# Kernel tuning notes

Hardware: AMD Instinct MI355X
Metric: run time of the kernel (lower is better)

## Reference

```python
import jax, jax.numpy as jnp
import numpy as np

EPS = 1e-6  # flax LayerNorm default

def _layer_norm(x, scale, bias):
    mu = jnp.mean(x, axis=-1, keepdims=True)
    var = jnp.mean(jnp.square(x - mu), axis=-1, keepdims=True)
    return (x - mu) * jax.lax.rsqrt(var + EPS) * scale + bias

def setup_inputs() -> dict:
    key = jax.random.key(0)
    ks = jax.random.split(key, 8)
    B, S, D_in, D_h, D_out, N = 4, 2048, 1024, 2048, 1024, 6
    init = lambda k, shape, fan_in: jax.random.normal(k, shape, jnp.float32) / np.sqrt(fan_in)
    return {
        "x": jax.random.normal(ks[0], (B, S, D_in), jnp.float32),
        "ln1_scale": jnp.ones((D_in,), jnp.float32),
        "ln1_bias": jnp.zeros((D_in,), jnp.float32),
        "w1": init(ks[1], (D_in, D_h), D_in),
        "b1": jnp.zeros((D_h,), jnp.float32),
        "block_ln_scales": jnp.ones((N, D_h), jnp.float32),
        "block_ln_biases": jnp.zeros((N, D_h), jnp.float32),
        "block_ws": init(ks[2], (N, D_h, D_h), D_h),
        "block_bs": jnp.zeros((N, D_h), jnp.float32),
        "ln2_scale": jnp.ones((D_h,), jnp.float32),
        "ln2_bias": jnp.zeros((D_h,), jnp.float32),
        "w2": init(ks[3], (D_h, D_out), D_h),
        "b2": jnp.zeros((D_out,), jnp.float32),
    }

def reference(x, ln1_scale, ln1_bias, w1, b1, block_ln_scales, block_ln_biases,
              block_ws, block_bs, ln2_scale, ln2_bias, w2, b2):
    # stem: LN -> Linear -> SiLU
    h = _layer_norm(x, ln1_scale, ln1_bias)
    h = jax.nn.silu(jnp.einsum('bsd,dh->bsh', h, w1) + b1)

    # residual blocks via scan over stacked params
    def block(h, params):
        s, b, w, lb = params
        y = _layer_norm(h, s, b)
        y = jax.nn.silu(jnp.einsum('bsh,hk->bsk', y, w) + lb)
        return h + y, None

    h, _ = jax.lax.scan(block, h, (block_ln_scales, block_ln_biases, block_ws, block_bs))

    # head: LN -> Linear
    h = _layer_norm(h, ln2_scale, ln2_bias)
    return jnp.einsum('bsh,ho->bso', h, w2) + b2
```

## Files before the change

kernel.cpp:

```cpp
#include <hip/hip_runtime.h>
#include <hip/hip_bf16.h>

typedef short short8 __attribute__((ext_vector_type(8)));
typedef float f32x4 __attribute__((ext_vector_type(4)));

#define AS1(p) ((const __attribute__((address_space(1))) void*)(p))
#define AS3(p) ((__attribute__((address_space(3))) void*)(p))

__device__ __forceinline__ ushort f2bf(float f) {
  __hip_bfloat16 h = __float2bfloat16(f);
  return *reinterpret_cast<const ushort*>(&h);
}
__device__ __forceinline__ float bfu2f(ushort u) {
  unsigned int x = ((unsigned int)u) << 16;
  float f;
  __builtin_memcpy(&f, &x, 4);
  return f;
}
__device__ __forceinline__ float silu_f(float v) { return v / (1.f + __expf(-v)); }

template<int NV>
__global__ __launch_bounds__(256) void ln_bf16_k(
    const float* __restrict__ in, const float* __restrict__ sc,
    const float* __restrict__ bi, ushort* __restrict__ out)
{
  const int D = NV * 1024;
  const long row = blockIdx.x;
  const int tx = threadIdx.x;
  const float* p = in + row * (long)D;
  float4 v[NV];
  float s = 0.f, s2 = 0.f;
#pragma unroll
  for (int t = 0; t < NV; ++t) {
    v[t] = *reinterpret_cast<const float4*>(p + t * 1024 + tx * 4);
    s  += v[t].x + v[t].y + v[t].z + v[t].w;
    s2 += v[t].x * v[t].x + v[t].y * v[t].y + v[t].z * v[t].z + v[t].w * v[t].w;
  }
#pragma unroll
  for (int o = 1; o < 64; o <<= 1) { s += __shfl_xor(s, o); s2 += __shfl_xor(s2, o); }
  __shared__ float red[2][4];
  const int wave = tx >> 6;
  if ((tx & 63) == 0) { red[0][wave] = s; red[1][wave] = s2; }
  __syncthreads();
  s  = red[0][0] + red[0][1] + red[0][2] + red[0][3];
  s2 = red[1][0] + red[1][1] + red[1][2] + red[1][3];
  const float mu   = s / D;
  const float rstd = rsqrtf(s2 / D - mu * mu + 1e-6f);
#pragma unroll
  for (int t = 0; t < NV; ++t) {
    const int d = t * 1024 + tx * 4;
    float4 g = *reinterpret_cast<const float4*>(sc + d);
    float4 b = *reinterpret_cast<const float4*>(bi + d);
    ushort4 o;
    o.x = f2bf((v[t].x - mu) * rstd * g.x + b.x);
    o.y = f2bf((v[t].y - mu) * rstd * g.y + b.y);
    o.z = f2bf((v[t].z - mu) * rstd * g.z + b.z);
    o.w = f2bf((v[t].w - mu) * rstd * g.w + b.w);
    *reinterpret_cast<ushort4*>(out + row * (long)D + d) = o;
  }
}

__global__ __launch_bounds__(256) void ln_stats_k(
    const ushort* __restrict__ in, float2* __restrict__ stats)
{
  const long row = blockIdx.x;
  const int tx = threadIdx.x;
  short8 v8 = *reinterpret_cast<const short8*>(in + row * 2048 + tx * 8);
  float s = 0.f, s2 = 0.f;
#pragma unroll
  for (int j = 0; j < 8; ++j) {
    const float v = bfu2f((ushort)v8[j]);
    s += v; s2 += v * v;
  }
#pragma unroll
  for (int o = 1; o < 64; o <<= 1) { s += __shfl_xor(s, o); s2 += __shfl_xor(s2, o); }
  __shared__ float red[2][4];
  const int wave = tx >> 6;
  if ((tx & 63) == 0) { red[0][wave] = s; red[1][wave] = s2; }
  __syncthreads();
  if (tx == 0) {
    s  = red[0][0] + red[0][1] + red[0][2] + red[0][3];
    s2 = red[1][0] + red[1][1] + red[1][2] + red[1][3];
    const float mu   = s * (1.f / 2048.f);
    const float rstd = rsqrtf(s2 * (1.f / 2048.f) - mu * mu + 1e-6f);
    stats[row] = make_float2(mu * rstd, rstd);
  }
}

__global__ __launch_bounds__(256) void transpose_bf16_k(
    const float* __restrict__ in, ushort* __restrict__ out, int K, int N)
{
  __shared__ float tile[64][65];
  const int k0 = blockIdx.y * 64, n0 = blockIdx.x * 64;
  const int tx = threadIdx.x, ty = threadIdx.y;
#pragma unroll
  for (int r = ty; r < 64; r += 4)
    tile[r][tx] = in[(long)(k0 + r) * N + n0 + tx];
  __syncthreads();
#pragma unroll
  for (int r = ty; r < 64; r += 4)
    out[(long)(n0 + r) * K + k0 + tx] = f2bf(tile[tx][r]);
}

__global__ __launch_bounds__(256) void transpose_scale_k(
    const float* __restrict__ in, const float* __restrict__ g,
    const float* __restrict__ beta, ushort* __restrict__ out,
    float2* __restrict__ uvw, int K, int N)
{
  __shared__ float tile[64][65];
  const int k0 = blockIdx.y * 64, n0 = blockIdx.x * 64;
  const int tx = threadIdx.x, ty = threadIdx.y;
  float pu = 0.f, pv = 0.f;
#pragma unroll
  for (int r = ty; r < 64; r += 4) {
    const float w  = in[(long)(k0 + r) * N + n0 + tx];
    const float ws = g[k0 + r] * w;
    tile[r][tx] = ws;
    pu += ws;
    pv += beta[k0 + r] * w;
  }
  atomicAdd(&uvw[n0 + tx].x, pu);
  atomicAdd(&uvw[n0 + tx].y, pv);
  __syncthreads();
#pragma unroll
  for (int r = ty; r < 64; r += 4)
    out[(long)(n0 + r) * K + k0 + tx] = f2bf(tile[tx][r]);
}

#define STG(gsrc, ldst)                                                          \
  __builtin_amdgcn_global_load_lds(AS1(gsrc),          AS3(ldst),          16, 0, 0); \
  __builtin_amdgcn_global_load_lds(AS1((gsrc) + offQ), AS3((ldst) + 8192), 16, 0, 0)

#define ldsA(B, H) (ldsW + (B) * 65536 + (H) * 16384)
#define ldsB(B, H) (ldsW + (B) * 65536 + 32768 + (H) * 16384)

#define RD_AF(DB, MH, KS)                                                       \
  _Pragma("unroll") for (int i_ = 0; i_ < 4; ++i_)                              \
    af[i_] = *(const short8*)(smem + (DB) * 65536 + aOff + ((MH) * 4 + i_) * 2048 + rdk[(KS)])

#define RD_BF(DST, DB, KS)                                                      \
  _Pragma("unroll") for (int j_ = 0; j_ < 4; ++j_)                              \
    DST[j_] = *(const short8*)(smem + (DB) * 65536 + bOff + j_ * 2048 + rdk[(KS)])

#define MFMA16(MH, BFR)                                                         \
  _Pragma("unroll") for (int i_ = 0; i_ < 4; ++i_)                              \
  _Pragma("unroll") for (int j_ = 0; j_ < 4; ++j_)                              \
    acc[(MH) * 4 + i_][j_] = __builtin_amdgcn_mfma_f32_16x16x32_bf16(           \
        af[i_], BFR[j_], acc[(MH) * 4 + i_], j_[0] * 0 + acc[(MH) * 4 + i_][j_], 0, 0, 0)

#undef MFMA16
#define MFMA16(MH, BFR)                                                         \
  _Pragma("unroll") for (int i_ = 0; i_ < 4; ++i_)                              \
  _Pragma("unroll") for (int j_ = 0; j_ < 4; ++j_)                              \
    acc[(MH) * 4 + i_][j_] = __builtin_amdgcn_mfma_f32_16x16x32_bf16(           \
        af[i_], BFR[j_], acc[(MH) * 4 + i_][j_], 0, 0, 0)

#define BARRIER __builtin_amdgcn_s_barrier()
#define LGKM0 do { asm volatile("s_waitcnt lgkmcnt(0)");                        \
                   __builtin_amdgcn_sched_barrier(0); } while (0)
#define W4 do { asm volatile("s_waitcnt vmcnt(4)" ::: "memory");                \
                __builtin_amdgcn_sched_barrier(0); } while (0)
#define W0 do { asm volatile("s_waitcnt vmcnt(0)" ::: "memory");                \
                __builtin_amdgcn_sched_barrier(0); } while (0)
#define WN do {} while (0)

#define DO_TILE(DB, S1, AO, S2, BO, WAITE)                                      \
  RD_AF(DB, 0, 0);                                                              \
  RD_BF(bf0, DB, 0);                                                            \
  RD_BF(bf1, DB, 1);                                                            \
  if (S1) { STG(aP + (AO), ldsA((DB) ^ 1, 0));                                  \
            STG(aP + (AO) + offH, ldsA((DB) ^ 1, 1)); }                         \
  BARRIER; LGKM0;                                                               \
  __builtin_amdgcn_s_setprio(1); MFMA16(0, bf0); __builtin_amdgcn_s_setprio(0); \
  BARRIER;                                                                      \
  RD_AF(DB, 1, 0);                                                              \
  if (S2) { STG(bP + (BO), ldsB(DB, 0)); }                                      \
  BARRIER; LGKM0;                                                               \
  __builtin_amdgcn_s_setprio(1); MFMA16(1, bf0); __builtin_amdgcn_s_setprio(0); \
  BARRIER;                                                                      \
  RD_AF(DB, 0, 1);                                                              \
  if (S2) { STG(bP + (BO) + offH, ldsB(DB, 1)); }                               \
  BARRIER; LGKM0;                                                               \
  __builtin_amdgcn_s_setprio(1); MFMA16(0, bf1); __builtin_amdgcn_s_setprio(0); \
  BARRIER;                                                                      \
  RD_AF(DB, 1, 1);                                                              \
  BARRIER; LGKM0;                                                               \
  __builtin_amdgcn_s_setprio(1); MFMA16(1, bf1); __builtin_amdgcn_s_setprio(0); \
  WAITE;                                                                        \
  BARRIER;

template<int MODE>
__global__ __launch_bounds__(512, 2) void gemm256_k(
    const ushort* __restrict__ A, const ushort* __restrict__ Bt,
    const float* __restrict__ bias, const float2* __restrict__ stats,
    const float2* __restrict__ uvw, const ushort* __restrict__ Rin,
    void* __restrict__ Cv, int M, int N, int K)
{
  extern __shared__ char smem[];
  const int tid = threadIdx.x;
  const int lane = tid & 63, wid = tid >> 6;
  const int wr = wid >> 2, wc = wid & 3;
  const int nbx = N >> 8;

  int bid;
  {
    const int b = blockIdx.x;
    const int cpx = gridDim.x >> 3;
    bid = (b & 7) * cpx + (b >> 3);
  }
  const int bx = bid % nbx, by = bid / nbx;
  const long m0 = (long)by << 8, n0 = (long)bx << 8;

  const int srow = tid >> 3;
  const int scol = (((tid & 7) * 16) ^ (((tid >> 3) & 7) << 4)) >> 1;
  const ushort* aP = A  + (m0 + srow) * (long)K + scol;
  const ushort* bP = Bt + (n0 + srow) * (long)K + scol;
  const long offH = 128L * K, offQ = 64L * K;
  char* ldsW = smem + wid * 1024;

  int rdk[2];
  rdk[0] = (((lane >> 4) * 16)     ) ^ ((lane & 7) << 4);
  rdk[1] = (((lane >> 4) * 16) + 64) ^ ((lane & 7) << 4);
  const int aOff = wr * 16384 + (lane & 15) * 128;
  const int bOff = 32768 + (wc >> 1) * 16384 + ((wc & 1) * 64 + (lane & 15)) * 128;

  f32x4 acc[8][4] = {};
  const int NT = K >> 6;

  STG(aP,      ldsA(0, 0));  STG(aP + offH,      ldsA(0, 1));
  STG(bP,      ldsB(0, 0));  STG(bP + offH,      ldsB(0, 1));
  STG(bP + 64, ldsB(1, 0));  STG(bP + 64 + offH, ldsB(1, 1));
  W4;
  BARRIER;

  short8 af[4], bf0[4], bf1[4];
  for (int t = 0; t < NT - 2; t += 2) {
    DO_TILE(0, 1,  64, 1, 128, W4)
    DO_TILE(1, 1, 128, 1, 192, W4)
    aP += 128; bP += 128;
  }
  DO_TILE(0, 1, 64, 0, 0, W0)
  DO_TILE(1, 0,  0, 0, 0, WN)

  if (MODE == 0) {
#pragma unroll
    for (int j = 0; j < 4; ++j) {
      const long col = n0 + wc * 64 + j * 16 + (lane & 15);
      const float bj = bias[col];
#pragma unroll
      for (int i = 0; i < 8; ++i) {
        const long rowb = m0 + wr * 128 + i * 16 + ((lane >> 4) << 2);
#pragma unroll
        for (int r = 0; r < 4; ++r) {
          const float v = acc[i][j][r] + bj;
          ((ushort*)Cv)[(rowb + r) * N + col] = f2bf(silu_f(v));
        }
      }
    }
  } else {
    float2 uvv[4];
    float  bj4[4];
    long   col4[4];
#pragma unroll
    for (int j = 0; j < 4; ++j) {
      col4[j] = n0 + wc * 64 + j * 16 + (lane & 15);
      uvv[j]  = uvw[col4[j]];
      bj4[j]  = bias[col4[j]];
    }
#pragma unroll
    for (int i = 0; i < 8; ++i) {
      const long rowb = m0 + wr * 128 + i * 16 + ((lane >> 4) << 2);
#pragma unroll
      for (int r = 0; r < 4; ++r) {
        const long row = rowb + r;
        const float2 ms = stats[row];
#pragma unroll
        for (int j = 0; j < 4; ++j) {
          const float v = ms.y * acc[i][j][r] - ms.x * uvv[j].x + uvv[j].y + bj4[j];
          const long idx = row * N + col4[j];
          if (MODE == 3) {
            ((ushort*)Cv)[idx] = f2bf(bfu2f(Rin[idx]) + silu_f(v));
          } else {
            ((float*)Cv)[idx] = v;
          }
        }
      }
    }
  }
}

extern "C" void kernel_launch(void* const* d_in, const int* in_sizes, int n_in,
                              void* d_out, int out_size, void* d_ws, size_t ws_size,
                              hipStream_t stream) {
  const float* x     = (const float*)d_in[0];
  const float* ln1_s = (const float*)d_in[1];
  const float* ln1_b = (const float*)d_in[2];
  const float* w1    = (const float*)d_in[3];
  const float* b1    = (const float*)d_in[4];
  const float* bln_s = (const float*)d_in[5];
  const float* bln_b = (const float*)d_in[6];
  const float* bws   = (const float*)d_in[7];
  const float* bbs   = (const float*)d_in[8];
  const float* ln2_s = (const float*)d_in[9];
  const float* ln2_b = (const float*)d_in[10];
  const float* w2    = (const float*)d_in[11];
  const float* b2    = (const float*)d_in[12];
  float* out = (float*)d_out;

  const int M = 8192;
  char* ws = (char*)d_ws;
  ushort* h0   = (ushort*)ws;
  ushort* h1   = (ushort*)(ws + 33554432);
  ushort* Abf  = h1;
  ushort* wt   = (ushort*)(ws + 67108864);
  float2* uvw  = (float2*)(ws + 125829120);
  float2* stats = (float2*)(ws + 125829120 + 114688);
  const long W1T = 0;
  const long BLK = 2097152;
  const long W2T = BLK + 6L * 4194304;

  (void)hipFuncSetAttribute((const void*)gemm256_k<0>,
      hipFuncAttributeMaxDynamicSharedMemorySize, 131072);
  (void)hipFuncSetAttribute((const void*)gemm256_k<3>,
      hipFuncAttributeMaxDynamicSharedMemorySize, 131072);
  (void)hipFuncSetAttribute((const void*)gemm256_k<4>,
      hipFuncAttributeMaxDynamicSharedMemorySize, 131072);

  (void)hipMemsetAsync(uvw, 0, 7 * 2048 * sizeof(float2), stream);

  dim3 tb(64, 4);
  transpose_bf16_k<<<dim3(32, 16), tb, 0, stream>>>(w1, wt + W1T, 1024, 2048);
  for (int i = 0; i < 6; ++i)
    transpose_scale_k<<<dim3(32, 32), tb, 0, stream>>>(
        bws + (long)i * 2048 * 2048, bln_s + i * 2048, bln_b + i * 2048,
        wt + BLK + (long)i * 4194304, uvw + (long)i * 2048, 2048, 2048);
  transpose_scale_k<<<dim3(16, 32), tb, 0, stream>>>(
      w2, ln2_s, ln2_b, wt + W2T, uvw + 6L * 2048, 2048, 1024);

  ln_bf16_k<1><<<M, 256, 0, stream>>>(x, ln1_s, ln1_b, Abf);
  gemm256_k<0><<<32 * 8, 512, 131072, stream>>>(
      Abf, wt + W1T, b1, nullptr, nullptr, nullptr, (void*)h0, M, 2048, 1024);

  ushort* hin = h0;
  ushort* hout = h1;
  for (int i = 0; i < 6; ++i) {
    ln_stats_k<<<M, 256, 0, stream>>>(hin, stats);
    gemm256_k<3><<<32 * 8, 512, 131072, stream>>>(
        hin, wt + BLK + (long)i * 4194304, bbs + i * 2048, stats,
        uvw + (long)i * 2048, hin, (void*)hout, M, 2048, 2048);
    ushort* tmp = hin; hin = hout; hout = tmp;
  }

  ln_stats_k<<<M, 256, 0, stream>>>(hin, stats);
  gemm256_k<4><<<32 * 4, 512, 131072, stream>>>(
      hin, wt + W2T, b2, stats, uvw + 6L * 2048, nullptr, (void*)out, M, 1024, 2048);
}
```

Before: 694.4 us.

## Software-pipeline LDS fragment reads with MFMA and drop most per-tile barriers

```diff
diff --git a/kernel.cpp b/kernel.cpp
--- a/kernel.cpp
+++ b/kernel.cpp
@@ -134,58 +134,54 @@
 #define ldsA(B, H) (ldsW + (B) * 65536 + (H) * 16384)
 #define ldsB(B, H) (ldsW + (B) * 65536 + 32768 + (H) * 16384)
 
-#define RD_AF(DB, MH, KS)                                                       \
+#define RD_AF(DST, DB, MH, KS)                                                  \
   _Pragma("unroll") for (int i_ = 0; i_ < 4; ++i_)                              \
-    af[i_] = *(const short8*)(smem + (DB) * 65536 + aOff + ((MH) * 4 + i_) * 2048 + rdk[(KS)])
+    DST[i_] = *(const short8*)(smem + (DB) * 65536 + aOff + ((MH) * 4 + i_) * 2048 + rdk[(KS)])
 
 #define RD_BF(DST, DB, KS)                                                      \
   _Pragma("unroll") for (int j_ = 0; j_ < 4; ++j_)                              \
     DST[j_] = *(const short8*)(smem + (DB) * 65536 + bOff + j_ * 2048 + rdk[(KS)])
 
-#define MFMA16(MH, BFR)                                                         \
+#define MFMA16(AREG, MH, BREG)                                                  \
   _Pragma("unroll") for (int i_ = 0; i_ < 4; ++i_)                              \
   _Pragma("unroll") for (int j_ = 0; j_ < 4; ++j_)                              \
     acc[(MH) * 4 + i_][j_] = __builtin_amdgcn_mfma_f32_16x16x32_bf16(           \
-        af[i_], BFR[j_], acc[(MH) * 4 + i_], j_[0] * 0 + acc[(MH) * 4 + i_][j_], 0, 0, 0)
-
-#undef MFMA16
-#define MFMA16(MH, BFR)                                                         \
-  _Pragma("unroll") for (int i_ = 0; i_ < 4; ++i_)                              \
-  _Pragma("unroll") for (int j_ = 0; j_ < 4; ++j_)                              \
-    acc[(MH) * 4 + i_][j_] = __builtin_amdgcn_mfma_f32_16x16x32_bf16(           \
-        af[i_], BFR[j_], acc[(MH) * 4 + i_][j_], 0, 0, 0)
+        AREG[i_], BREG[j_], acc[(MH) * 4 + i_][j_], 0, 0, 0)
 
 #define BARRIER __builtin_amdgcn_s_barrier()
-#define LGKM0 do { asm volatile("s_waitcnt lgkmcnt(0)");                        \
-                   __builtin_amdgcn_sched_barrier(0); } while (0)
-#define W4 do { asm volatile("s_waitcnt vmcnt(4)" ::: "memory");                \
-                __builtin_amdgcn_sched_barrier(0); } while (0)
-#define W0 do { asm volatile("s_waitcnt vmcnt(0)" ::: "memory");                \
-                __builtin_amdgcn_sched_barrier(0); } while (0)
+#define SP1 __builtin_amdgcn_s_setprio(1)
+#define SP0 __builtin_amdgcn_s_setprio(0)
+#define SBAR __builtin_amdgcn_sched_barrier(0)
+#define LGKMW(N) do { asm volatile("s_waitcnt lgkmcnt(" #N ")"); SBAR; } while (0)
+#define W4 do { asm volatile("s_waitcnt vmcnt(4)" ::: "memory"); SBAR; } while (0)
+#define W0 do { asm volatile("s_waitcnt vmcnt(0)" ::: "memory"); SBAR; } while (0)
 #define WN do {} while (0)
 
 #define DO_TILE(DB, S1, AO, S2, BO, WAITE)                                      \
-  RD_AF(DB, 0, 0);                                                              \
-  RD_BF(bf0, DB, 0);                                                            \
-  RD_BF(bf1, DB, 1);                                                            \
+             \
+  RD_AF(afx, DB, 0, 0);                                                         \
+  RD_BF(bf, DB, 0);                                                             \
+  RD_AF(afy, DB, 1, 0);                                                         \
   if (S1) { STG(aP + (AO), ldsA((DB) ^ 1, 0));                                  \
             STG(aP + (AO) + offH, ldsA((DB) ^ 1, 1)); }                         \
-  BARRIER; LGKM0;                                                               \
-  __builtin_amdgcn_s_setprio(1); MFMA16(0, bf0); __builtin_amdgcn_s_setprio(0); \
-  BARRIER;                                                                      \
-  RD_AF(DB, 1, 0);                                                              \
-  if (S2) { STG(bP + (BO), ldsB(DB, 0)); }                                      \
-  BARRIER; LGKM0;                                                               \
-  __builtin_amdgcn_s_setprio(1); MFMA16(1, bf0); __builtin_amdgcn_s_setprio(0); \
-  BARRIER;                                                                      \
-  RD_AF(DB, 0, 1);                                                              \
-  if (S2) { STG(bP + (BO) + offH, ldsB(DB, 1)); }                               \
-  BARRIER; LGKM0;                                                               \
-  __builtin_amdgcn_s_setprio(1); MFMA16(0, bf1); __builtin_amdgcn_s_setprio(0); \
-  BARRIER;                                                                      \
-  RD_AF(DB, 1, 1);                                                              \
-  BARRIER; LGKM0;                                                               \
-  __builtin_amdgcn_s_setprio(1); MFMA16(1, bf1); __builtin_amdgcn_s_setprio(0); \
+  LGKMW(4);                                     \
+  SP1; MFMA16(afx, 0, bf); SP0;                                                 \
+                  \
+  RD_AF(afx, DB, 0, 1);                                                         \
+  LGKMW(4);                                      \
+  SP1; MFMA16(afy, 1, bf); SP0;                                                 \
+  RD_BF(bf, DB, 1);                                                             \
+  SBAR;                                                                         \
+                                 \
+  RD_AF(afy, DB, 1, 1);                                                         \
+  LGKMW(4);                                     \
+  SP1; MFMA16(afx, 0, bf); SP0;                                                 \
+  BARRIER;                                         \
+                  \
+  if (S2) { STG(bP + (BO), ldsB(DB, 0));                                        \
+            STG(bP + (BO) + offH, ldsB(DB, 1)); }                               \
+  LGKMW(0);                                                                     \
+  SP1; MFMA16(afy, 1, bf); SP0;                                                 \
   WAITE;                                                                        \
   BARRIER;
 
@@ -233,7 +229,7 @@
   W4;
   BARRIER;
 
-  short8 af[4], bf0[4], bf1[4];
+  short8 afx[4], afy[4], bf[4];
   for (int t = 0; t < NT - 2; t += 2) {
     DO_TILE(0, 1,  64, 1, 128, W4)
     DO_TILE(1, 1, 128, 1, 192, W4)
```

Result: no change. 693.1 us (-0.2%).
